# Optimization experiments

Measured on AMD Instinct MI355X. Metric: run time of the kernel, lower is better.

Reference implementation:

```python
import jax, jax.numpy as jnp
import numpy as np

N, IN_DIM, D, H, OUT = 4096, 512, 256, 256, 128


def setup_inputs() -> dict:
    key = jax.random.key(0)
    ks = jax.random.split(key, 12)
    s = 0.05
    x = jax.random.normal(ks[0], (N, IN_DIM), dtype=jnp.float32)
    # sparse-ish dense adjacency mask (avg degree ~80), int since only adj>0 is used
    adj = (jax.random.uniform(ks[1], (N, N)) < 0.02).astype(jnp.int32)
    return {
        "x": x,
        "adj": adj,
        "lin1_w": jax.random.normal(ks[2], (D, IN_DIM), dtype=jnp.float32) * s,
        "lin1_b": jax.random.normal(ks[3], (D,), dtype=jnp.float32) * s,
        "gat_W": jax.random.normal(ks[4], (D, D), dtype=jnp.float32) * s,
        "a_self": jax.random.normal(ks[5], (D,), dtype=jnp.float32) * s,
        "a_neigh": jax.random.normal(ks[6], (D,), dtype=jnp.float32) * s,
        "W_ih": jax.random.normal(ks[7], (4 * H, D), dtype=jnp.float32) * s,
        "W_hh": jax.random.normal(ks[8], (4 * H, H), dtype=jnp.float32) * s,
        "lin2_w": jax.random.normal(ks[9], (OUT, D), dtype=jnp.float32) * s,
        "lin2_b": jax.random.normal(ks[10], (OUT,), dtype=jnp.float32) * s,
    }


def reference(x, adj, lin1_w, lin1_b, gat_W, a_self, a_neigh, W_ih, W_hh, lin2_w, lin2_b):
    M = jnp.float32(0.2)        # scalar M passed by EWNELayer
    LRELU_SLOPE = 0.2           # alpha given to GraphAttentionLayer
    NEG_INF = jnp.float32(-9e15)

    # lin1
    x1 = x @ lin1_w.T + lin1_b                       # [N, D]

    # --- GraphAttentionLayer (DAEGC-style, dense adjacency mask) ---
    h = x1 @ gat_W                                   # [N, D]
    e = (h @ a_self)[:, None] + (h @ a_neigh)[None, :]  # [N, N]
    e = jax.nn.leaky_relu(e * M, LRELU_SLOPE)
    scores = jnp.where(adj > 0, e, NEG_INF)
    attn = jax.nn.softmax(scores, axis=1)            # [N, N]
    h_prime = attn @ h                               # [N, D]
    g = jnp.tanh(jax.nn.elu(h_prime))                # ELU (concat=True) then tanh

    # --- single-timestep LSTM, no bias, h0 = c0 = 0 ---
    h0 = jnp.zeros((N, H), dtype=g.dtype)
    c0 = jnp.zeros((N, H), dtype=g.dtype)
    gates = g @ W_ih.T + h0 @ W_hh.T                 # [N, 4H], torch order i,f,g,o
    i_g, f_g, g_g, o_g = jnp.split(gates, 4, axis=1)
    i_g = jax.nn.sigmoid(i_g)
    f_g = jax.nn.sigmoid(f_g)
    g_g = jnp.tanh(g_g)
    o_g = jax.nn.sigmoid(o_g)
    c1 = f_g * c0 + i_g * g_g
    h1 = o_g * jnp.tanh(c1)                          # [N, H]

    # lin2 -> normalize -> dot-product decode
    out = h1 @ lin2_w.T + lin2_b                     # [N, OUT]
    norm = jnp.maximum(jnp.linalg.norm(out, axis=1, keepdims=True), 1e-12)
    z = out / norm
    A_pred = jax.nn.sigmoid(z @ z.T)                 # [N, N]
    return A_pred, z, out
```

## Files before the change

### kernel.cpp

```cpp
#include <hip/hip_runtime.h>

#define NN_ 4096
#define IN_DIM_ 512
#define D_ 256
#define OUT_ 128

typedef unsigned short u16;
typedef unsigned int u32;
typedef __attribute__((ext_vector_type(8))) short short8;
typedef __attribute__((ext_vector_type(4))) float f32x4;
typedef __attribute__((ext_vector_type(4))) int i32x4;

union U16x8 { uint4 u4; short8 s8; };

__device__ __forceinline__ u16 f2bf(float f){
  u32 u = __builtin_bit_cast(u32, f);
  u = (u + 0x7FFFu + ((u >> 16) & 1u)) >> 16;
  return (u16)u;
}
__device__ __forceinline__ float bf2f(u16 u){ return __builtin_bit_cast(float, ((u32)u) << 16); }
__device__ __forceinline__ float sigm(float v){ return __fdividef(1.f, 1.f + __expf(-v)); }

__device__ __forceinline__ void mfma_mainloop(const u16* __restrict__ A,
    const u16* __restrict__ B, int K, int ldA, int ldB, int row0, int col0,
    uint4* As, uint4* Bs, f32x4 acc[4][4], int tid) {
  const int wave = tid >> 6, lane = tid & 63;
  const int wm = wave >> 1, wn = wave & 1;
  const int r16 = lane & 15, kg = lane >> 4;
  for (int k0 = 0; k0 < K; k0 += 64) {
    #pragma unroll
    for (int i = 0; i < 4; i++) {
      int id = tid + (i << 8);
      int r = id >> 3, cc = id & 7;
      As[(r << 3) + (cc ^ (r & 7))] = *(const uint4*)(A + (size_t)(row0 + r) * ldA + k0 + cc * 8);
      Bs[(r << 3) + (cc ^ (r & 7))] = *(const uint4*)(B + (size_t)(col0 + r) * ldB + k0 + cc * 8);
    }
    __syncthreads();
    #pragma unroll
    for (int ks = 0; ks < 2; ks++) {
      int kb = (ks << 2) + kg;
      U16x8 a[4], b[4];
      #pragma unroll
      for (int m2 = 0; m2 < 4; m2++) {
        int r = (wm << 6) + (m2 << 4) + r16;
        a[m2].u4 = As[(r << 3) + (kb ^ (r & 7))];
      }
      #pragma unroll
      for (int n2 = 0; n2 < 4; n2++) {
        int r = (wn << 6) + (n2 << 4) + r16;
        b[n2].u4 = Bs[(r << 3) + (kb ^ (r & 7))];
      }
      #pragma unroll
      for (int m2 = 0; m2 < 4; m2++)
        #pragma unroll
        for (int n2 = 0; n2 < 4; n2++)
          acc[m2][n2] = __builtin_amdgcn_mfma_f32_16x16x32_bf16(
              a[m2].s8, b[n2].s8, acc[m2][n2], 0, 0, 0);
    }
    __syncthreads();
  }
}

__global__ __launch_bounds__(256) void prep_kernel(
    const float* __restrict__ lin1_w, const float* __restrict__ gat_W,
    const float* __restrict__ lin1_b,
    u16* __restrict__ WcT_bf, float* __restrict__ bcomb) {
  __shared__ __align__(16) float sh[2 * 32 * 68];
  const int b = blockIdx.x, tid = threadIdx.x;
  if (b < 32) {
    float (*As)[68] = (float(*)[68])sh;
    float (*Bs)[68] = (float(*)[68])(sh + 32 * 68);
    int m0 = (b & 7) << 6, n0 = (b >> 3) << 6;
    const int tx = tid & 15, ty = tid >> 4;
    float acc[4][4] = {};
    for (int k0 = 0; k0 < 256; k0 += 32) {
      #pragma unroll
      for (int i = 0; i < 2; i++) {
        int id = tid + (i << 8);
        int kk = id >> 4, c4 = (id & 15) << 2;
        *(float4*)&As[kk][c4] = *(const float4*)(lin1_w + (size_t)(k0 + kk) * 512 + m0 + c4);
        *(float4*)&Bs[kk][c4] = *(const float4*)(gat_W + (size_t)(k0 + kk) * 256 + n0 + c4);
      }
      __syncthreads();
      #pragma unroll
      for (int kk = 0; kk < 32; kk++) {
        float4 av = *(const float4*)&As[kk][ty << 2];
        float4 bv = *(const float4*)&Bs[kk][tx << 2];
        float a_[4] = {av.x, av.y, av.z, av.w};
        float b_[4] = {bv.x, bv.y, bv.z, bv.w};
        #pragma unroll
        for (int r = 0; r < 4; r++)
          #pragma unroll
          for (int c = 0; c < 4; c++)
            acc[r][c] = __builtin_fmaf(a_[r], b_[c], acc[r][c]);
      }
      __syncthreads();
    }
    #pragma unroll
    for (int r = 0; r < 4; r++)
      #pragma unroll
      for (int c = 0; c < 4; c++)
        WcT_bf[(size_t)(n0 + (tx << 2) + c) * 512 + m0 + (ty << 2) + r] = f2bf(acc[r][c]);
  } else {
    float a = 0.f;
    #pragma unroll 8
    for (int d = 0; d < 256; d++)
      a = __builtin_fmaf(lin1_b[d], gat_W[(size_t)d * 256 + tid], a);
    bcomb[tid] = a;
  }
}

__global__ __launch_bounds__(256) void hgemm_st_kernel(const float* __restrict__ x,
    const u16* __restrict__ WcT, const float* __restrict__ bias,
    const float* __restrict__ a_self, const float* __restrict__ a_nei,
    const float* __restrict__ W_ih, const float* __restrict__ lin2_w,
    u16* __restrict__ h_bf, float* __restrict__ s, float* __restrict__ t,
    u16* __restrict__ Wih_bf, u16* __restrict__ l2w_bf) {
  __shared__ uint4 As[16 * 8];
  __shared__ uint4 Bs[256 * 8];
  __shared__ float sred[4][16];
  __shared__ float tred[4][16];
  const int tid = threadIdx.x;
  int b = blockIdx.x;
  if (b >= 256) {
    b -= 256;
    if (b < 256) {
      int r = (b << 2) + (tid >> 6);
      int grp = r >> 6, gate = (r >> 4) & 3, hcl = r & 15;
      int orig = gate * 256 + grp * 16 + hcl;
      int k = (tid & 63) << 2;
      float4 v = *(const float4*)(W_ih + (size_t)orig * 256 + k);
      ushort4 o = {f2bf(v.x), f2bf(v.y), f2bf(v.z), f2bf(v.w)};
      *(ushort4*)(Wih_bf + (size_t)r * 256 + k) = o;
    } else {
      int off = (b - 256) * 1024 + tid * 4;
      float4 v = *(const float4*)(lin2_w + off);
      ushort4 o = {f2bf(v.x), f2bf(v.y), f2bf(v.z), f2bf(v.w)};
      *(ushort4*)(l2w_bf + off) = o;
    }
    return;
  }
  const int row0 = b << 4;
  const int wave = tid >> 6, lane = tid & 63;
  const int r16 = lane & 15, kg = lane >> 4;
  f32x4 acc[4];
  #pragma unroll
  for (int n2 = 0; n2 < 4; n2++) acc[n2] = (f32x4){0.f,0.f,0.f,0.f};
  for (int k0 = 0; k0 < IN_DIM_; k0 += 64) {
    if (tid < 128) {
      int r = tid >> 3, cc = tid & 7;
      const float* src = x + (size_t)(row0 + r) * IN_DIM_ + k0 + cc * 8;
      float4 lo = *(const float4*)src;
      float4 hi = *(const float4*)(src + 4);
      u16 e[8] = {f2bf(lo.x), f2bf(lo.y), f2bf(lo.z), f2bf(lo.w),
                  f2bf(hi.x), f2bf(hi.y), f2bf(hi.z), f2bf(hi.w)};
      As[(r << 3) + (cc ^ (r & 7))] = *(uint4*)e;
    }
    #pragma unroll
    for (int i = 0; i < 8; i++) {
      int id = tid + (i << 8);
      int r = id >> 3, cc = id & 7;
      Bs[(r << 3) + (cc ^ (r & 7))] = *(const uint4*)(WcT + (size_t)r * IN_DIM_ + k0 + cc * 8);
    }
    __syncthreads();
    #pragma unroll
    for (int ks = 0; ks < 2; ks++) {
      int kb = (ks << 2) + kg;
      U16x8 a, bb[4];
      a.u4 = As[(r16 << 3) + (kb ^ (r16 & 7))];
      #pragma unroll
      for (int n2 = 0; n2 < 4; n2++) {
        int r = (wave << 6) + (n2 << 4) + r16;
        bb[n2].u4 = Bs[(r << 3) + (kb ^ (r & 7))];
      }
      #pragma unroll
      for (int n2 = 0; n2 < 4; n2++)
        acc[n2] = __builtin_amdgcn_mfma_f32_16x16x32_bf16(a.s8, bb[n2].s8, acc[n2], 0, 0, 0);
    }
    __syncthreads();
  }
  float ps[4] = {0.f,0.f,0.f,0.f}, pt[4] = {0.f,0.f,0.f,0.f};
  #pragma unroll
  for (int n2 = 0; n2 < 4; n2++) {
    int col = (wave << 6) + (n2 << 4) + r16;
    float as = a_self[col], an = a_nei[col], bs = bias[col];
    #pragma unroll
    for (int q = 0; q < 4; q++) {
      float v = acc[n2][q] + bs;
      h_bf[(size_t)(row0 + (kg << 2) + q) * D_ + col] = f2bf(v);
      ps[q] = __builtin_fmaf(v, as, ps[q]);
      pt[q] = __builtin_fmaf(v, an, pt[q]);
    }
  }
  #pragma unroll
  for (int q = 0; q < 4; q++) {
    #pragma unroll
    for (int off = 8; off; off >>= 1) {
      ps[q] += __shfl_xor(ps[q], off);
      pt[q] += __shfl_xor(pt[q], off);
    }
  }
  if (r16 == 0) {
    #pragma unroll
    for (int q = 0; q < 4; q++) {
      sred[wave][(kg << 2) + q] = ps[q];
      tred[wave][(kg << 2) + q] = pt[q];
    }
  }
  __syncthreads();
  if (tid < 16)
    s[row0 + tid] = sred[0][tid] + sred[1][tid] + sred[2][tid] + sred[3][tid];
  else if (tid < 32)
    t[row0 + tid - 16] = tred[0][tid-16] + tred[1][tid-16] + tred[2][tid-16] + tred[3][tid-16];
}

#define MAXN 512
__global__ __launch_bounds__(256) void attn3_kernel(const int* __restrict__ adj,
    const u16* __restrict__ h_bf, const float* __restrict__ s,
    const float* __restrict__ t, u16* __restrict__ g_bf) {
  __shared__ int nidx[MAXN];
  __shared__ float ne[MAXN];
  __shared__ float red[4][256];
  __shared__ int wtot[4];
  __shared__ float reds[4];
  const int tid = threadIdx.x;
  const int row = blockIdx.x;
  const int lane = tid & 63, wave = tid >> 6;
  const i32x4* arow = (const i32x4*)(adj + (size_t)row * NN_);
  i32x4 a4[4];
  #pragma unroll
  for (int i = 0; i < 4; i++) a4[i] = __builtin_nontemporal_load(&arow[(i << 8) + tid]);
  int vals[16];
  #pragma unroll
  for (int i = 0; i < 4; i++)
    #pragma unroll
    for (int q = 0; q < 4; q++) vals[(i << 2) + q] = a4[i][q];
  int c = 0;
  #pragma unroll
  for (int q = 0; q < 16; q++) c += (vals[q] > 0);
  int pref = c;
  #pragma unroll
  for (int off = 1; off < 64; off <<= 1) {
    int u = __shfl_up(pref, off);
    if (lane >= off) pref += u;
  }
  if (lane == 63) wtot[wave] = pref;
  __syncthreads();
  int woff = 0;
  #pragma unroll
  for (int w = 0; w < 4; w++) woff += (w < wave) ? wtot[w] : 0;
  int n = wtot[0] + wtot[1] + wtot[2] + wtot[3];
  float si = s[row];
  int p = woff + pref - c;
  float ls = 0.f;
  #pragma unroll
  for (int i = 0; i < 4; i++)
    #pragma unroll
    for (int q = 0; q < 4; q++) {
      if (vals[(i << 2) + q] > 0) {
        int j = (i << 10) + (tid << 2) + q;
        float e = 0.2f * (si + t[j]);
        e = e > 0.f ? e : 0.2f * e;
        float wgt = __expf(e);
        if (p < MAXN) { nidx[p] = j; ne[p] = wgt; ls += wgt; }
        p++;
      }
    }
  if (n > MAXN) n = MAXN;
  #pragma unroll
  for (int off = 32; off; off >>= 1) ls += __shfl_xor(ls, off);
  if (lane == 0) reds[wave] = ls;
  __syncthreads();
  float S = reds[0] + reds[1] + reds[2] + reds[3];
  const int hl = lane & 31, ksel = lane >> 5;
  float acc[8] = {0.f, 0.f, 0.f, 0.f, 0.f, 0.f, 0.f, 0.f};
  #pragma unroll 4
  for (int k = (wave << 1) + ksel; k < n; k += 8) {
    float wgt = ne[k];
    int j = nidx[k];
    U16x8 hv; hv.u4 = *(const uint4*)(h_bf + ((size_t)j << 8) + (hl << 3));
    #pragma unroll
    for (int q = 0; q < 8; q++)
      acc[q] = __builtin_fmaf(wgt, bf2f((u16)hv.s8[q]), acc[q]);
  }
  #pragma unroll
  for (int q = 0; q < 8; q++) acc[q] += __shfl_down(acc[q], 32);
  if (lane < 32) {
    #pragma unroll
    for (int q = 0; q < 8; q++) red[wave][(hl << 3) + q] = acc[q];
  }
  __syncthreads();
  float hp;
  if (n > 0) {
    hp = (red[0][tid] + red[1][tid] + red[2][tid] + red[3][tid]) / S;
  } else {
    float a2 = 0.f;
    for (int j = 0; j < NN_; j++) a2 += bf2f(h_bf[((size_t)j << 8) + tid]);
    hp = a2 / NN_;
  }
  float el = hp > 0.f ? hp : __expf(hp) - 1.f;
  g_bf[((size_t)row << 8) + tid] = f2bf(tanhf(el));
}

__global__ __launch_bounds__(256) void gates_lstm_kernel(const u16* __restrict__ A,
    const u16* __restrict__ B, u16* __restrict__ h1b) {
  __shared__ uint4 As[128 * 8];
  __shared__ uint4 Bs[128 * 8];
  const int tid = threadIdx.x;
  const int row0 = blockIdx.y << 7, col0 = blockIdx.x << 7;
  f32x4 acc[4][4];
  #pragma unroll
  for (int m2 = 0; m2 < 4; m2++)
    #pragma unroll
    for (int n2 = 0; n2 < 4; n2++) acc[m2][n2] = (f32x4){0.f,0.f,0.f,0.f};
  mfma_mainloop(A, B, D_, D_, D_, row0, col0, As, Bs, acc, tid);
  const int wave = tid >> 6, lane = tid & 63;
  const int r16 = lane & 15, kg = lane >> 4;
  const int orow = row0 + ((wave >> 1) << 6);
  const int hc = ((blockIdx.x << 1) + (wave & 1)) * 16 + r16;
  #pragma unroll
  for (int m2 = 0; m2 < 4; m2++)
    #pragma unroll
    for (int q = 0; q < 4; q++) {
      size_t grow = orow + (m2 << 4) + (kg << 2) + q;
      float ig = acc[m2][0][q], gg = acc[m2][2][q], og = acc[m2][3][q];
      float c1 = sigm(ig) * tanhf(gg);
      h1b[grow * D_ + hc] = f2bf(sigm(og) * tanhf(c1));
    }
}

__global__ __launch_bounds__(256) void lin2f_kernel(const u16* __restrict__ A,
    const u16* __restrict__ B, const float* __restrict__ bias,
    float* __restrict__ out, float* __restrict__ z, u16* __restrict__ zb) {
  __shared__ uint4 As[16 * 8];
  __shared__ uint4 Bs[128 * 8];
  __shared__ float ssred[4][16];
  const int tid = threadIdx.x;
  const int wave = tid >> 6, lane = tid & 63;
  const int r16 = lane & 15, kg = lane >> 4;
  const int row0 = blockIdx.x << 4;
  f32x4 acc[2];
  acc[0] = (f32x4){0.f,0.f,0.f,0.f}; acc[1] = (f32x4){0.f,0.f,0.f,0.f};
  for (int k0 = 0; k0 < D_; k0 += 64) {
    if (tid < 128) {
      int r = tid >> 3, cc = tid & 7;
      As[(r << 3) + (cc ^ (r & 7))] = *(const uint4*)(A + (size_t)(row0 + r) * D_ + k0 + cc * 8);
    }
    #pragma unroll
    for (int i = 0; i < 4; i++) {
      int id = tid + (i << 8);
      int r = id >> 3, cc = id & 7;
      Bs[(r << 3) + (cc ^ (r & 7))] = *(const uint4*)(B + (size_t)r * D_ + k0 + cc * 8);
    }
    __syncthreads();
    #pragma unroll
    for (int ks = 0; ks < 2; ks++) {
      int kb = (ks << 2) + kg;
      U16x8 a, bb[2];
      a.u4 = As[(r16 << 3) + (kb ^ (r16 & 7))];
      #pragma unroll
      for (int n2 = 0; n2 < 2; n2++) {
        int r = (wave << 5) + (n2 << 4) + r16;
        bb[n2].u4 = Bs[(r << 3) + (kb ^ (r & 7))];
      }
      #pragma unroll
      for (int n2 = 0; n2 < 2; n2++)
        acc[n2] = __builtin_amdgcn_mfma_f32_16x16x32_bf16(a.s8, bb[n2].s8, acc[n2], 0, 0, 0);
    }
    __syncthreads();
  }
  float v[2][4], ss[4];
  #pragma unroll
  for (int q = 0; q < 4; q++) ss[q] = 0.f;
  #pragma unroll
  for (int n2 = 0; n2 < 2; n2++) {
    int col = (wave << 5) + (n2 << 4) + r16;
    float bs = bias[col];
    #pragma unroll
    for (int q = 0; q < 4; q++) {
      float vv = acc[n2][q] + bs;
      v[n2][q] = vv;
      ss[q] = __builtin_fmaf(vv, vv, ss[q]);
    }
  }
  #pragma unroll
  for (int q = 0; q < 4; q++)
    #pragma unroll
    for (int off = 8; off; off >>= 1) ss[q] += __shfl_xor(ss[q], off);
  if (r16 == 0) {
    #pragma unroll
    for (int q = 0; q < 4; q++) ssred[wave][(kg << 2) + q] = ss[q];
  }
  __syncthreads();
  #pragma unroll
  for (int q = 0; q < 4; q++) {
    int rrow = (kg << 2) + q;
    float tot = ssred[0][rrow] + ssred[1][rrow] + ssred[2][rrow] + ssred[3][rrow];
    float inv = __fdividef(1.f, fmaxf(sqrtf(tot), 1e-12f));
    size_t grow = row0 + rrow;
    #pragma unroll
    for (int n2 = 0; n2 < 2; n2++) {
      int col = (wave << 5) + (n2 << 4) + r16;
      float vv = v[n2][q], zz = vv * inv;
      __builtin_nontemporal_store(vv, &out[grow * OUT_ + col]);
      __builtin_nontemporal_store(zz, &z[grow * OUT_ + col]);
      zb[grow * OUT_ + col] = f2bf(zz);
    }
  }
}

__global__ __launch_bounds__(256) void decode_kernel(const u16* __restrict__ zb,
    float* __restrict__ C) {
  __shared__ uint4 As[128 * 8];
  __shared__ uint4 Bs[128 * 8];
  const int tid = threadIdx.x;
  const int row0 = blockIdx.y << 7, col0 = blockIdx.x << 7;
  f32x4 acc[4][4];
  #pragma unroll
  for (int m2 = 0; m2 < 4; m2++)
    #pragma unroll
    for (int n2 = 0; n2 < 4; n2++) acc[m2][n2] = (f32x4){0.f,0.f,0.f,0.f};
  mfma_mainloop(zb, zb, OUT_, OUT_, OUT_, row0, col0, As, Bs, acc, tid);
  const int wave = tid >> 6, lane = tid & 63;
  const int r16 = lane & 15, kg = lane >> 4;
  const int orow = row0 + ((wave >> 1) << 6), ocol = col0 + ((wave & 1) << 6);
  #pragma unroll
  for (int m2 = 0; m2 < 4; m2++)
    #pragma unroll
    for (int n2 = 0; n2 < 4; n2++)
      #pragma unroll
      for (int q = 0; q < 4; q++) {
        size_t gr = orow + (m2 << 4) + (kg << 2) + q;
        int gc = ocol + (n2 << 4) + r16;
        __builtin_nontemporal_store(sigm(acc[m2][n2][q]), &C[gr * NN_ + gc]);
      }
}

extern "C" void kernel_launch(void* const* d_in, const int* in_sizes, int n_in,
                              void* d_out, int out_size, void* d_ws, size_t ws_size,
                              hipStream_t stream) {
  const float* x      = (const float*)d_in[0];
  const int*   adj    = (const int*)  d_in[1];
  const float* lin1_w = (const float*)d_in[2];
  const float* lin1_b = (const float*)d_in[3];
  const float* gat_W  = (const float*)d_in[4];
  const float* a_self = (const float*)d_in[5];
  const float* a_nei  = (const float*)d_in[6];
  const float* W_ih   = (const float*)d_in[7];
  const float* lin2_w = (const float*)d_in[9];
  const float* lin2_b = (const float*)d_in[10];

  float* A_pred = (float*)d_out;
  float* z_out  = A_pred + (size_t)NN_ * NN_;
  float* out_o  = z_out + (size_t)NN_ * OUT_;

  char* w = (char*)d_ws;
  u16* h_bf   = (u16*)w;
  u16* g_bf   = (u16*)(w + (2u << 20));
  u16* h1_bf  = (u16*)(w + (4u << 20));
  u16* zb     = (u16*)(w + (6u << 20));
  u16* Wih_bf = (u16*)(w + (7u << 20));
  u16* WcT_bf = (u16*)(w + (7u << 20) + (512u << 10));
  u16* l2w_bf = (u16*)(w + (7u << 20) + (768u << 10));
  float* bcomb= (float*)(w + (7u << 20) + (832u << 10));
  float* s    = (float*)(w + (7u << 20) + (896u << 10));
  float* t    = (float*)(w + (7u << 20) + (960u << 10));

  prep_kernel<<<dim3(33), dim3(256), 0, stream>>>(
      lin1_w, gat_W, lin1_b, WcT_bf, bcomb);
  hgemm_st_kernel<<<dim3(544), dim3(256), 0, stream>>>(
      x, WcT_bf, bcomb, a_self, a_nei, W_ih, lin2_w, h_bf, s, t, Wih_bf, l2w_bf);
  attn3_kernel<<<dim3(4096), dim3(256), 0, stream>>>(adj, h_bf, s, t, g_bf);
  gates_lstm_kernel<<<dim3(8, 32), dim3(256), 0, stream>>>(g_bf, Wih_bf, h1_bf);
  lin2f_kernel<<<dim3(256), dim3(256), 0, stream>>>(h1_bf, l2w_bf, lin2_b, out_o, z_out, zb);
  decode_kernel<<<dim3(32, 32), dim3(256), 0, stream>>>(zb, A_pred);
}
```

Before: 90.61 us.

## Fuse LSTM gate GEMM with lin2/normalize and drop unused forget-gate weights

Combines the LSTM gate GEMM and the lin2+normalize kernel into one kernel per 16-row tile. The h1 activations stay in LDS instead of going through global memory. The W_ih repack now keeps only the i, g and o gate rows, since the forget gate is multiplied by c0=0, which removes a quarter of the gate GEMM work. It also replaces the nontemporal stores for out, z and A_pred with normal stores. The trade-off is a 256-block launch where each block re-streams all 768 gate-weight rows, giving less parallelism than the old 8x32-tile gate GEMM.

Measured after the change: 115.3 us. 1.27x slower.

```diff
diff --git a/kernel.cpp b/kernel.cpp
--- a/kernel.cpp
+++ b/kernel.cpp
@@ -115,7 +115,7 @@
     const float* __restrict__ a_self, const float* __restrict__ a_nei,
     const float* __restrict__ W_ih, const float* __restrict__ lin2_w,
     u16* __restrict__ h_bf, float* __restrict__ s, float* __restrict__ t,
-    u16* __restrict__ Wih_bf, u16* __restrict__ l2w_bf) {
+    u16* __restrict__ Wihp_bf, u16* __restrict__ l2w_bf) {
   __shared__ uint4 As[16 * 8];
   __shared__ uint4 Bs[256 * 8];
   __shared__ float sred[4][16];
@@ -124,16 +124,18 @@
   int b = blockIdx.x;
   if (b >= 256) {
     b -= 256;
-    if (b < 256) {
+    if (b < 192) {
       int r = (b << 2) + (tid >> 6);
-      int grp = r >> 6, gate = (r >> 4) & 3, hcl = r & 15;
+      int grp = r / 48, rem = r - grp * 48;
+      int gidx = rem >> 4, hcl = rem & 15;
+      int gate = (gidx == 0) ? 0 : ((gidx == 1) ? 2 : 3);
       int orig = gate * 256 + grp * 16 + hcl;
       int k = (tid & 63) << 2;
       float4 v = *(const float4*)(W_ih + (size_t)orig * 256 + k);
       ushort4 o = {f2bf(v.x), f2bf(v.y), f2bf(v.z), f2bf(v.w)};
-      *(ushort4*)(Wih_bf + (size_t)r * 256 + k) = o;
+      *(ushort4*)(Wihp_bf + (size_t)r * 256 + k) = o;
     } else {
-      int off = (b - 256) * 1024 + tid * 4;
+      int off = (b - 192) * 1024 + tid * 4;
       float4 v = *(const float4*)(lin2_w + off);
       ushort4 o = {f2bf(v.x), f2bf(v.y), f2bf(v.z), f2bf(v.w)};
       *(ushort4*)(l2w_bf + off) = o;
@@ -302,70 +304,94 @@
   g_bf[((size_t)row << 8) + tid] = f2bf(tanhf(el));
 }
 
-__global__ __launch_bounds__(256) void gates_lstm_kernel(const u16* __restrict__ A,
-    const u16* __restrict__ B, u16* __restrict__ h1b) {
-  __shared__ uint4 As[128 * 8];
-  __shared__ uint4 Bs[128 * 8];
-  const int tid = threadIdx.x;
-  const int row0 = blockIdx.y << 7, col0 = blockIdx.x << 7;
-  f32x4 acc[4][4];
-  #pragma unroll
-  for (int m2 = 0; m2 < 4; m2++)
-    #pragma unroll
-    for (int n2 = 0; n2 < 4; n2++) acc[m2][n2] = (f32x4){0.f,0.f,0.f,0.f};
-  mfma_mainloop(A, B, D_, D_, D_, row0, col0, As, Bs, acc, tid);
-  const int wave = tid >> 6, lane = tid & 63;
-  const int r16 = lane & 15, kg = lane >> 4;
-  const int orow = row0 + ((wave >> 1) << 6);
-  const int hc = ((blockIdx.x << 1) + (wave & 1)) * 16 + r16;
-  #pragma unroll
-  for (int m2 = 0; m2 < 4; m2++)
-    #pragma unroll
-    for (int q = 0; q < 4; q++) {
-      size_t grow = orow + (m2 << 4) + (kg << 2) + q;
-      float ig = acc[m2][0][q], gg = acc[m2][2][q], og = acc[m2][3][q];
-      float c1 = sigm(ig) * tanhf(gg);
-      h1b[grow * D_ + hc] = f2bf(sigm(og) * tanhf(c1));
-    }
-}
-
-__global__ __launch_bounds__(256) void lin2f_kernel(const u16* __restrict__ A,
-    const u16* __restrict__ B, const float* __restrict__ bias,
-    float* __restrict__ out, float* __restrict__ z, u16* __restrict__ zb) {
-  __shared__ uint4 As[16 * 8];
-  __shared__ uint4 Bs[128 * 8];
+__global__ __launch_bounds__(256) void gates_lin2_kernel(const u16* __restrict__ g_bf,
+    const u16* __restrict__ Wihp, const u16* __restrict__ l2w,
+    const float* __restrict__ bias, float* __restrict__ out,
+    float* __restrict__ z, u16* __restrict__ zb) {
+  __shared__ uint4 As[16 * 32];
+  __shared__ uint4 Bs[192 * 8];
+  __shared__ u16 h1s[16 * 256];
   __shared__ float ssred[4][16];
   const int tid = threadIdx.x;
   const int wave = tid >> 6, lane = tid & 63;
   const int r16 = lane & 15, kg = lane >> 4;
   const int row0 = blockIdx.x << 4;
-  f32x4 acc[2];
-  acc[0] = (f32x4){0.f,0.f,0.f,0.f}; acc[1] = (f32x4){0.f,0.f,0.f,0.f};
+  #pragma unroll
+  for (int i = 0; i < 2; i++) {
+    int e = tid + (i << 8);
+    int r = e >> 5, kb = e & 31;
+    As[(r << 5) + (kb ^ (r & 7))] = *(const uint4*)(g_bf + (size_t)(row0 + r) * D_ + kb * 8);
+  }
+  f32x4 acc[4][3];
+  #pragma unroll
+  for (int cc = 0; cc < 4; cc++)
+    #pragma unroll
+    for (int n2 = 0; n2 < 3; n2++) acc[cc][n2] = (f32x4){0.f,0.f,0.f,0.f};
+  for (int cc = 0; cc < 4; cc++) {
+    for (int k0 = 0; k0 < D_; k0 += 64) {
+      #pragma unroll
+      for (int i = 0; i < 6; i++) {
+        int e = tid + (i << 8);
+        int r = e >> 3, c8 = e & 7;
+        Bs[(r << 3) + (c8 ^ (r & 7))] = *(const uint4*)(Wihp + (size_t)(cc * 192 + r) * D_ + k0 + c8 * 8);
+      }
+      __syncthreads();
+      #pragma unroll
+      for (int ks = 0; ks < 2; ks++) {
+        int kbi = (k0 >> 3) + (ks << 2) + kg;
+        int kb8 = (ks << 2) + kg;
+        U16x8 a, bb[3];
+        a.u4 = As[(r16 << 5) + (kbi ^ (r16 & 7))];
+        #pragma unroll
+        for (int n2 = 0; n2 < 3; n2++) {
+          int r = wave * 48 + n2 * 16 + r16;
+          bb[n2].u4 = Bs[(r << 3) + (kb8 ^ (r & 7))];
+        }
+        #pragma unroll
+        for (int n2 = 0; n2 < 3; n2++)
+          acc[cc][n2] = __builtin_amdgcn_mfma_f32_16x16x32_bf16(a.s8, bb[n2].s8, acc[cc][n2], 0, 0, 0);
+      }
+      __syncthreads();
+    }
+  }
+  #pragma unroll
+  for (int cc = 0; cc < 4; cc++) {
+    int hc = ((cc << 2) + wave) * 16 + r16;
+    int u = hc >> 3, sub = hc & 7;
+    #pragma unroll
+    for (int q = 0; q < 4; q++) {
+      int r = (kg << 2) + q;
+      float i_ = acc[cc][0][q], g_ = acc[cc][1][q], o_ = acc[cc][2][q];
+      float c1 = sigm(i_) * tanhf(g_);
+      h1s[((r << 5) + (u ^ (r & 7))) * 8 + sub] = f2bf(sigm(o_) * tanhf(c1));
+    }
+  }
+  __syncthreads();
+  const uint4* h1v = (const uint4*)h1s;
+  f32x4 acc2[2];
+  acc2[0] = (f32x4){0.f,0.f,0.f,0.f}; acc2[1] = (f32x4){0.f,0.f,0.f,0.f};
   for (int k0 = 0; k0 < D_; k0 += 64) {
-    if (tid < 128) {
-      int r = tid >> 3, cc = tid & 7;
-      As[(r << 3) + (cc ^ (r & 7))] = *(const uint4*)(A + (size_t)(row0 + r) * D_ + k0 + cc * 8);
-    }
     #pragma unroll
     for (int i = 0; i < 4; i++) {
-      int id = tid + (i << 8);
-      int r = id >> 3, cc = id & 7;
-      Bs[(r << 3) + (cc ^ (r & 7))] = *(const uint4*)(B + (size_t)r * D_ + k0 + cc * 8);
+      int e = tid + (i << 8);
+      int r = e >> 3, c8 = e & 7;
+      Bs[(r << 3) + (c8 ^ (r & 7))] = *(const uint4*)(l2w + (size_t)r * D_ + k0 + c8 * 8);
     }
     __syncthreads();
     #pragma unroll
     for (int ks = 0; ks < 2; ks++) {
-      int kb = (ks << 2) + kg;
+      int kbi = (k0 >> 3) + (ks << 2) + kg;
+      int kb8 = (ks << 2) + kg;
       U16x8 a, bb[2];
-      a.u4 = As[(r16 << 3) + (kb ^ (r16 & 7))];
+      a.u4 = h1v[(r16 << 5) + (kbi ^ (r16 & 7))];
       #pragma unroll
       for (int n2 = 0; n2 < 2; n2++) {
         int r = (wave << 5) + (n2 << 4) + r16;
-        bb[n2].u4 = Bs[(r << 3) + (kb ^ (r & 7))];
+        bb[n2].u4 = Bs[(r << 3) + (kb8 ^ (r & 7))];
       }
       #pragma unroll
       for (int n2 = 0; n2 < 2; n2++)
-        acc[n2] = __builtin_amdgcn_mfma_f32_16x16x32_bf16(a.s8, bb[n2].s8, acc[n2], 0, 0, 0);
+        acc2[n2] = __builtin_amdgcn_mfma_f32_16x16x32_bf16(a.s8, bb[n2].s8, acc2[n2], 0, 0, 0);
     }
     __syncthreads();
   }
@@ -378,7 +404,7 @@
     float bs = bias[col];
     #pragma unroll
     for (int q = 0; q < 4; q++) {
-      float vv = acc[n2][q] + bs;
+      float vv = acc2[n2][q] + bs;
       v[n2][q] = vv;
       ss[q] = __builtin_fmaf(vv, vv, ss[q]);
     }
@@ -402,8 +428,8 @@
     for (int n2 = 0; n2 < 2; n2++) {
       int col = (wave << 5) + (n2 << 4) + r16;
       float vv = v[n2][q], zz = vv * inv;
-      __builtin_nontemporal_store(vv, &out[grow * OUT_ + col]);
-      __builtin_nontemporal_store(zz, &z[grow * OUT_ + col]);
+      out[grow * OUT_ + col] = vv;
+      z[grow * OUT_ + col] = zz;
       zb[grow * OUT_ + col] = f2bf(zz);
     }
   }
@@ -432,7 +458,7 @@
       for (int q = 0; q < 4; q++) {
         size_t gr = orow + (m2 << 4) + (kg << 2) + q;
         int gc = ocol + (n2 << 4) + r16;
-        __builtin_nontemporal_store(sigm(acc[m2][n2][q]), &C[gr * NN_ + gc]);
+        C[gr * NN_ + gc] = sigm(acc[m2][n2][q]);
       }
 }
 
@@ -455,23 +481,22 @@
   float* out_o  = z_out + (size_t)NN_ * OUT_;
 
   char* w = (char*)d_ws;
-  u16* h_bf   = (u16*)w;
-  u16* g_bf   = (u16*)(w + (2u << 20));
-  u16* h1_bf  = (u16*)(w + (4u << 20));
-  u16* zb     = (u16*)(w + (6u << 20));
-  u16* Wih_bf = (u16*)(w + (7u << 20));
-  u16* WcT_bf = (u16*)(w + (7u << 20) + (512u << 10));
-  u16* l2w_bf = (u16*)(w + (7u << 20) + (768u << 10));
-  float* bcomb= (float*)(w + (7u << 20) + (832u << 10));
-  float* s    = (float*)(w + (7u << 20) + (896u << 10));
-  float* t    = (float*)(w + (7u << 20) + (960u << 10));
+  u16* h_bf    = (u16*)w;
+  u16* g_bf    = (u16*)(w + (2u << 20));
+  u16* zb      = (u16*)(w + (4u << 20));
+  u16* Wihp_bf = (u16*)(w + (5u << 20));
+  u16* WcT_bf  = (u16*)(w + (5u << 20) + (384u << 10));
+  u16* l2w_bf  = (u16*)(w + (5u << 20) + (640u << 10));
+  float* bcomb = (float*)(w + (5u << 20) + (704u << 10));
+  float* s     = (float*)(w + (5u << 20) + (768u << 10));
+  float* t     = (float*)(w + (5u << 20) + (832u << 10));
 
   prep_kernel<<<dim3(33), dim3(256), 0, stream>>>(
       lin1_w, gat_W, lin1_b, WcT_bf, bcomb);
-  hgemm_st_kernel<<<dim3(544), dim3(256), 0, stream>>>(
-      x, WcT_bf, bcomb, a_self, a_nei, W_ih, lin2_w, h_bf, s, t, Wih_bf, l2w_bf);
+  hgemm_st_kernel<<<dim3(480), dim3(256), 0, stream>>>(
+      x, WcT_bf, bcomb, a_self, a_nei, W_ih, lin2_w, h_bf, s, t, Wihp_bf, l2w_bf);
   attn3_kernel<<<dim3(4096), dim3(256), 0, stream>>>(adj, h_bf, s, t, g_bf);
-  gates_lstm_kernel<<<dim3(8, 32), dim3(256), 0, stream>>>(g_bf, Wih_bf, h1_bf);
-  lin2f_kernel<<<dim3(256), dim3(256), 0, stream>>>(h1_bf, l2w_bf, lin2_b, out_o, z_out, zb);
+  gates_lin2_kernel<<<dim3(256), dim3(256), 0, stream>>>(
+      g_bf, Wihp_bf, l2w_bf, lin2_b, out_o, z_out, zb);
   decode_kernel<<<dim3(32, 32), dim3(256), 0, stream>>>(zb, A_pred);
 }
```
